# Kernel optimization log

Hardware: AMD Instinct MI355X
Metric: run time of the kernel (lower is better)

The kernel has to match this reference:

```python
import jax, jax.numpy as jnp
import numpy as np

T, B, F, H = 2048, 50, 750, 100  # time, batch(seen by LSTM), input feat, hidden
OUT = 2

def setup_inputs() -> dict:
    key = jax.random.key(0)
    ks = jax.random.split(key, 7)
    s = 1.0 / np.sqrt(H)
    u = lambda k, shape: jax.random.uniform(k, shape, jnp.float32, -s, s)
    return {
        "x": jax.random.normal(ks[0], (T, B, F), jnp.float32),
        "W_ih": u(ks[1], (4 * H, F)),
        "W_hh": u(ks[2], (4 * H, H)),
        "b_ih": u(ks[3], (4 * H,)),
        "b_hh": u(ks[4], (4 * H,)),
        "fc_W": u(ks[5], (OUT, B * H)),
        "fc_b": u(ks[6], (OUT,)),
    }

def reference(x, W_ih, W_hh, b_ih, b_hh, fc_W, fc_b):
    # PyTorch LSTM (batch_first=False): scan over dim0. Gate order: i, f, g, o.
    # Precompute input projections for all steps at once: (T, B, 4H)
    x_proj = jnp.einsum('tbf,gf->tbg', x, W_ih) + b_ih + b_hh

    def step(carry, xp):
        h, c = carry                      # (B, H) each
        gates = xp + h @ W_hh.T           # (B, 4H)
        i, f, g, o = jnp.split(gates, 4, axis=-1)
        i = jax.nn.sigmoid(i)
        f = jax.nn.sigmoid(f)
        g = jnp.tanh(g)
        o = jax.nn.sigmoid(o)
        c = f * c + i * g
        h = o * jnp.tanh(c)
        return (h, c), h

    h0 = jnp.zeros((B, H), x.dtype)
    c0 = jnp.zeros((B, H), x.dtype)
    _, hs = jax.lax.scan(step, (h0, c0), x_proj)  # hs: (T, B, H)
    flat = hs.reshape(hs.shape[0], -1)            # (T, B*H) == (T, 5000)
    return flat @ fc_W.T + fc_b                   # (T, 2)
```

## Files before the change

### kernel.cpp

```cpp
#include <hip/hip_runtime.h>

#define T_DIM 2048
#define B_DIM 50
#define F_DIM 750
#define H_DIM 100
#define G4    400
#define M_DIM (T_DIM * B_DIM)
#define KPAD  768

typedef __attribute__((ext_vector_type(8))) short short8v;
typedef __attribute__((ext_vector_type(4))) float f32x4;

__device__ __forceinline__ float fast_rcp(float x) { return __builtin_amdgcn_rcpf(x); }
__device__ __forceinline__ float sigm_f(float x) {
    return fast_rcp(1.0f + __expf(-x));
}
__device__ __forceinline__ float tanh_f(float x) {
    return 1.0f - 2.0f * fast_rcp(__expf(2.0f * x) + 1.0f);
}

__device__ __forceinline__ unsigned short f2bf_rne(float f) {
    unsigned int u = __float_as_uint(f);
    u = (u + 0x7FFFu + ((u >> 16) & 1u)) >> 16;
    return (unsigned short)u;
}
__device__ __forceinline__ float bf2f(unsigned short h) {
    return __uint_as_float(((unsigned int)h) << 16);
}

template <int CTRL>
__device__ __forceinline__ float qperm(float x) {
    return __int_as_float(__builtin_amdgcn_mov_dpp(__float_as_int(x), CTRL, 0xF, 0xF, false));
}

__global__ __launch_bounds__(256) void wconv(
    const float* __restrict__ W,
    unsigned short* __restrict__ Whi,
    unsigned short* __restrict__ Wlo)
{
    int i = blockIdx.x * 256 + threadIdx.x;
    if (i >= G4 * KPAD) return;
    int g = i / KPAD, k = i - g * KPAD;
    float v = (k < F_DIM) ? W[g * F_DIM + k] : 0.f;
    unsigned short h = f2bf_rne(v);
    Whi[i] = h;
    Wlo[i] = f2bf_rne(v - bf2f(h));
}

__global__ __launch_bounds__(256, 2) void xproj_mfma(
    const float* __restrict__ x,
    const unsigned short* __restrict__ Whi,
    const unsigned short* __restrict__ Wlo,
    const float* __restrict__ bih,
    const float* __restrict__ bhh,
    float* __restrict__ xp)
{
    const int m0   = blockIdx.x * 64;
    const int tid  = threadIdx.x;
    const int lane = tid & 63;
    const int w    = tid >> 6;
    const int fr   = lane & 15;
    const int fk   = (lane >> 4) * 8;

    __shared__ unsigned short Ahi[2][64][40];
    __shared__ unsigned short Alo[2][64][40];

    f32x4 acc[4][7];
    #pragma unroll
    for (int s = 0; s < 4; ++s)
        #pragma unroll
        for (int t = 0; t < 7; ++t)
            acc[s][t] = (f32x4){0.f, 0.f, 0.f, 0.f};

    float bias_t[7];
    #pragma unroll
    for (int tt = 0; tt < 7; ++tt) {
        const int nt = w + 4 * tt;
        if (nt < 25) {
            const int n = nt * 16 + fr;
            bias_t[tt] = bih[n] + bhh[n];
        } else bias_t[tt] = 0.f;
    }

    const int sr = tid >> 2;
    const int sc = (tid & 3) * 8;
    const float* xrow = x + (size_t)(m0 + sr) * F_DIM;

    float f[8];

    #define STAGE_LOAD(KS)                                                     \
    {                                                                          \
        const int kg = (KS) * 32 + sc;                                         \
        _Pragma("unroll")                                                      \
        for (int i = 0; i < 8; i += 2) {                                       \
            if (kg + i + 1 < F_DIM) {                                          \
                float2 v = *reinterpret_cast<const float2*>(&xrow[kg + i]);    \
                f[i] = v.x; f[i + 1] = v.y;                                    \
            } else {                                                           \
                f[i]     = (kg + i < F_DIM) ? xrow[kg + i] : 0.f;              \
                f[i + 1] = 0.f;                                                \
            }                                                                  \
        }                                                                      \
    }

    #define STAGE_WRITE(NB)                                                    \
    {                                                                          \
        short8v vh, vl;                                                        \
        _Pragma("unroll")                                                      \
        for (int i = 0; i < 8; ++i) {                                          \
            unsigned int u = __float_as_uint(f[i]);                            \
            vh[i] = (short)(u >> 16);                                          \
            float r = f[i] - __uint_as_float(u & 0xffff0000u);                 \
            vl[i] = (short)(__float_as_uint(r) >> 16);                         \
        }                                                                      \
        *reinterpret_cast<short8v*>(&Ahi[NB][sr][sc]) = vh;                    \
        *reinterpret_cast<short8v*>(&Alo[NB][sr][sc]) = vl;                    \
    }

    STAGE_LOAD(0);
    STAGE_WRITE(0);
    asm volatile("s_waitcnt lgkmcnt(0)\ns_barrier" ::: "memory");

    for (int s = 0; s < 24; ++s) {
        const int cur = s & 1;
        short8v ah[4], al[4];
        #pragma unroll
        for (int st = 0; st < 4; ++st) {
            ah[st] = *reinterpret_cast<const short8v*>(&Ahi[cur][st * 16 + fr][fk]);
            al[st] = *reinterpret_cast<const short8v*>(&Alo[cur][st * 16 + fr][fk]);
        }

        if (s < 23) STAGE_LOAD(s + 1);

        const int kb = s * 32 + fk;
        #pragma unroll
        for (int tt = 0; tt < 7; ++tt) {
            const int nt = w + 4 * tt;
            if (nt < 25) {
                const int n = nt * 16 + fr;
                const short8v bh = *reinterpret_cast<const short8v*>(&Whi[n * KPAD + kb]);
                const short8v bl = *reinterpret_cast<const short8v*>(&Wlo[n * KPAD + kb]);
                #pragma unroll
                for (int st = 0; st < 4; ++st) {
                    acc[st][tt] = __builtin_amdgcn_mfma_f32_16x16x32_bf16(ah[st], bh, acc[st][tt], 0, 0, 0);
                    acc[st][tt] = __builtin_amdgcn_mfma_f32_16x16x32_bf16(ah[st], bl, acc[st][tt], 0, 0, 0);
                    acc[st][tt] = __builtin_amdgcn_mfma_f32_16x16x32_bf16(al[st], bh, acc[st][tt], 0, 0, 0);
                }
            }
        }

        if (s < 23) STAGE_WRITE(cur ^ 1);
        asm volatile("s_waitcnt lgkmcnt(0)\ns_barrier" ::: "memory");
    }

    #pragma unroll
    for (int tt = 0; tt < 7; ++tt) {
        const int nt = w + 4 * tt;
        if (nt < 25) {
            const int n = nt * 16 + fr;
            #pragma unroll
            for (int st = 0; st < 4; ++st) {
                #pragma unroll
                for (int r = 0; r < 4; ++r) {
                    const int m = m0 + st * 16 + (lane >> 4) * 4 + r;
                    xp[(size_t)m * G4 + n] = acc[st][tt][r] + bias_t[tt];
                }
            }
        }
    }
    #undef STAGE_LOAD
    #undef STAGE_WRITE
}

__global__ __launch_bounds__(448, 1) void lstm_scan(
    const float* __restrict__ xp,
    const float* __restrict__ Whh,
    float* __restrict__ hs)
{
    const int b   = blockIdx.x;
    const int tid = threadIdx.x;
    const int q   = tid & 3;
    const int j   = tid >> 2;
    const int jc  = (j < H_DIM) ? j : (H_DIM - 1);
    const int row = q * H_DIM + jc;

    __shared__ __align__(16) float hbuf[2][112];

    float w[4][28];
    #pragma unroll
    for (int g = 0; g < 4; ++g) {
        const size_t base = (size_t)(g * H_DIM + jc) * H_DIM + 25 * q;
        #pragma unroll
        for (int r = 0; r < 25; ++r) w[g][r] = Whh[base + r];
        w[g][25] = w[g][26] = w[g][27] = 0.f;
    }
    if (tid < 112) { hbuf[0][tid] = 0.f; hbuf[1][tid] = 0.f; }

    const int hpos = (jc / 25) * 28 + (jc % 25);
    const bool writer = (q == 0) && (j < H_DIM);

    const float s_act = (q == 2) ? 2.0f : 1.0f;
    const float nsl2  = -s_act * 1.44269504088896f;
    const float nsm1  = 1.0f - s_act;

    float c = 0.f;
    const float* xp_ptr = xp + (size_t)b * G4 + row;
    float*       hs_ptr = hs + (size_t)b * H_DIM + j;
    float xpv = *xp_ptr;
    __syncthreads();

    int p = 0;
    for (int t = 0; t < T_DIM; ++t) {
        float xp_next = 0.f;
        if (t != T_DIM - 1) {
            xp_ptr += B_DIM * G4;
            xp_next = *xp_ptr;
        }

        float ac0 = (q == 0) ? xpv : 0.f;
        float ac1 = (q == 1) ? xpv : 0.f;
        float ac2 = (q == 2) ? xpv : 0.f;
        float ac3 = (q == 3) ? xpv : 0.f;
        #pragma unroll
        for (int k4 = 0; k4 < 7; ++k4) {
            float4 hv = *reinterpret_cast<const float4*>(&hbuf[p][28 * q + 4 * k4]);
            ac0 = fmaf(w[0][4 * k4 + 0], hv.x, ac0);
            ac0 = fmaf(w[0][4 * k4 + 1], hv.y, ac0);
            ac0 = fmaf(w[0][4 * k4 + 2], hv.z, ac0);
            ac0 = fmaf(w[0][4 * k4 + 3], hv.w, ac0);
            ac1 = fmaf(w[1][4 * k4 + 0], hv.x, ac1);
            ac1 = fmaf(w[1][4 * k4 + 1], hv.y, ac1);
            ac1 = fmaf(w[1][4 * k4 + 2], hv.z, ac1);
            ac1 = fmaf(w[1][4 * k4 + 3], hv.w, ac1);
            ac2 = fmaf(w[2][4 * k4 + 0], hv.x, ac2);
            ac2 = fmaf(w[2][4 * k4 + 1], hv.y, ac2);
            ac2 = fmaf(w[2][4 * k4 + 2], hv.z, ac2);
            ac2 = fmaf(w[2][4 * k4 + 3], hv.w, ac2);
            ac3 = fmaf(w[3][4 * k4 + 0], hv.x, ac3);
            ac3 = fmaf(w[3][4 * k4 + 1], hv.y, ac3);
            ac3 = fmaf(w[3][4 * k4 + 2], hv.z, ac3);
            ac3 = fmaf(w[3][4 * k4 + 3], hv.w, ac3);
        }
        ac0 += qperm<0xB1>(ac0);
        ac1 += qperm<0xB1>(ac1);
        ac2 += qperm<0xB1>(ac2);
        ac3 += qperm<0xB1>(ac3);
        ac0 += qperm<0x4E>(ac0);
        ac1 += qperm<0x4E>(ac1);
        ac2 += qperm<0x4E>(ac2);
        ac3 += qperm<0x4E>(ac3);

        float pre = ac0;
        pre = (q == 1) ? ac1 : pre;
        pre = (q == 2) ? ac2 : pre;
        pre = (q == 3) ? ac3 : pre;
        float act = fmaf(s_act, fast_rcp(1.0f + __builtin_amdgcn_exp2f(nsl2 * pre)), nsm1);

        float i_ = qperm<0x00>(act);
        float f_ = qperm<0x55>(act);
        float g_ = qperm<0xAA>(act);
        float o_ = qperm<0xFF>(act);

        c = fmaf(f_, c, i_ * g_);
        const float h = o_ * tanh_f(c);

        if (writer) {
            hbuf[p ^ 1][hpos] = h;
            *hs_ptr = h;
        }
        hs_ptr += B_DIM * H_DIM;
        asm volatile("s_waitcnt lgkmcnt(0)\ns_barrier" ::: "memory");
        p ^= 1;
        xpv = xp_next;
    }
}

__global__ __launch_bounds__(256) void fc_kernel(
    const float* __restrict__ hs,
    const float* __restrict__ fcW,
    const float* __restrict__ fcb,
    float* __restrict__ out)
{
    const int t   = blockIdx.x;
    const int tid = threadIdx.x;

    float p0 = 0.f, p1 = 0.f;
    for (int k = tid * 4; k < 5000; k += 1024) {
        const float4 hv = *reinterpret_cast<const float4*>(&hs[(size_t)t * 5000 + k]);
        const float4 w0 = *reinterpret_cast<const float4*>(&fcW[k]);
        const float4 w1 = *reinterpret_cast<const float4*>(&fcW[5000 + k]);
        p0 += hv.x * w0.x + hv.y * w0.y + hv.z * w0.z + hv.w * w0.w;
        p1 += hv.x * w1.x + hv.y * w1.y + hv.z * w1.z + hv.w * w1.w;
    }
    #pragma unroll
    for (int off = 32; off > 0; off >>= 1) {
        p0 += __shfl_xor(p0, off);
        p1 += __shfl_xor(p1, off);
    }
    __shared__ float red[8];
    const int wv = tid >> 6;
    if ((tid & 63) == 0) { red[wv * 2] = p0; red[wv * 2 + 1] = p1; }
    __syncthreads();
    if (tid == 0) {
        out[2 * t]     = fcb[0] + red[0] + red[2] + red[4] + red[6];
        out[2 * t + 1] = fcb[1] + red[1] + red[3] + red[5] + red[7];
    }
}

extern "C" void kernel_launch(void* const* d_in, const int* in_sizes, int n_in,
                              void* d_out, int out_size, void* d_ws, size_t ws_size,
                              hipStream_t stream) {
    const float* x   = (const float*)d_in[0];
    const float* Wih = (const float*)d_in[1];
    const float* Whh = (const float*)d_in[2];
    const float* bih = (const float*)d_in[3];
    const float* bhh = (const float*)d_in[4];
    const float* fcW = (const float*)d_in[5];
    const float* fcb = (const float*)d_in[6];
    float* out = (float*)d_out;

    char* ws = (char*)d_ws;
    float*          xp  = (float*)ws;
    unsigned short* Whi = (unsigned short*)(ws + (size_t)M_DIM * G4 * 4);
    unsigned short* Wlo = Whi + (size_t)G4 * KPAD;
    float*          hs  = (float*)((char*)(Wlo + (size_t)G4 * KPAD));

    wconv<<<(G4 * KPAD + 255) / 256, 256, 0, stream>>>(Wih, Whi, Wlo);

    xproj_mfma<<<M_DIM / 64, 256, 0, stream>>>(x, Whi, Wlo, bih, bhh, xp);

    lstm_scan<<<B_DIM, 448, 0, stream>>>(xp, Whh, hs);

    fc_kernel<<<T_DIM, 256, 0, stream>>>(hs, fcW, fcb, out);
}
```

Baseline: 1.493 ms.

## Enlarge xproj tile to 128 rows, pack LSTM scan FMAs, prefetch two steps

The input-projection GEMM now runs 512-thread blocks covering 128 rows, so two wave groups share each W_ih column tile. This halves the number of W reads per output row. The LSTM scan stores recurrent weights as float2 pairs and uses elementwise vector FMA, aiming at packed FP32 FMA instructions that shorten the serial per-step dot product. It also prefetches xp two timesteps ahead to hide global load latency on the recurrence. The larger GEMM block and the STAGE_LOAD indexing, which is partly hidden, must cover 128 rows correctly, and both changes raise register and LDS pressure.

```diff
diff --git a/kernel.cpp b/kernel.cpp
--- a/kernel.cpp
+++ b/kernel.cpp
@@ -10,11 +10,9 @@
 
 typedef __attribute__((ext_vector_type(8))) short short8v;
 typedef __attribute__((ext_vector_type(4))) float f32x4;
+typedef __attribute__((ext_vector_type(2))) float f32x2;
 
 __device__ __forceinline__ float fast_rcp(float x) { return __builtin_amdgcn_rcpf(x); }
-__device__ __forceinline__ float sigm_f(float x) {
-    return fast_rcp(1.0f + __expf(-x));
-}
 __device__ __forceinline__ float tanh_f(float x) {
     return 1.0f - 2.0f * fast_rcp(__expf(2.0f * x) + 1.0f);
 }
@@ -47,7 +45,7 @@
     Wlo[i] = f2bf_rne(v - bf2f(h));
 }
 
-__global__ __launch_bounds__(256, 2) void xproj_mfma(
+__global__ __launch_bounds__(512, 1) void xproj_mfma(
     const float* __restrict__ x,
     const unsigned short* __restrict__ Whi,
     const unsigned short* __restrict__ Wlo,
@@ -55,15 +53,17 @@
     const float* __restrict__ bhh,
     float* __restrict__ xp)
 {
-    const int m0   = blockIdx.x * 64;
+    const int m0   = blockIdx.x * 128;
     const int tid  = threadIdx.x;
     const int lane = tid & 63;
     const int w    = tid >> 6;
+    const int rb   = (w >> 2) * 64;
+    const int wc   = w & 3;
     const int fr   = lane & 15;
     const int fk   = (lane >> 4) * 8;
 
-    __shared__ unsigned short Ahi[2][64][40];
-    __shared__ unsigned short Alo[2][64][40];
+    __shared__ unsigned short Ahi[2][128][40];
+    __shared__ unsigned short Alo[2][128][40];
 
     f32x4 acc[4][7];
     #pragma unroll
@@ -75,7 +75,7 @@
     float bias_t[7];
     #pragma unroll
     for (int tt = 0; tt < 7; ++tt) {
-        const int nt = w + 4 * tt;
+        const int nt = wc + 4 * tt;
         if (nt < 25) {
             const int n = nt * 16 + fr;
             bias_t[tt] = bih[n] + bhh[n];
@@ -126,8 +126,8 @@
         short8v ah[4], al[4];
         #pragma unroll
         for (int st = 0; st < 4; ++st) {
-            ah[st] = *reinterpret_cast<const short8v*>(&Ahi[cur][st * 16 + fr][fk]);
-            al[st] = *reinterpret_cast<const short8v*>(&Alo[cur][st * 16 + fr][fk]);
+            ah[st] = *reinterpret_cast<const short8v*>(&Ahi[cur][rb + st * 16 + fr][fk]);
+            al[st] = *reinterpret_cast<const short8v*>(&Alo[cur][rb + st * 16 + fr][fk]);
         }
 
         if (s < 23) STAGE_LOAD(s + 1);
@@ -135,7 +135,7 @@
         const int kb = s * 32 + fk;
         #pragma unroll
         for (int tt = 0; tt < 7; ++tt) {
-            const int nt = w + 4 * tt;
+            const int nt = wc + 4 * tt;
             if (nt < 25) {
                 const int n = nt * 16 + fr;
                 const short8v bh = *reinterpret_cast<const short8v*>(&Whi[n * KPAD + kb]);
@@ -155,14 +155,14 @@
 
     #pragma unroll
     for (int tt = 0; tt < 7; ++tt) {
-        const int nt = w + 4 * tt;
+        const int nt = wc + 4 * tt;
         if (nt < 25) {
             const int n = nt * 16 + fr;
             #pragma unroll
             for (int st = 0; st < 4; ++st) {
                 #pragma unroll
                 for (int r = 0; r < 4; ++r) {
-                    const int m = m0 + st * 16 + (lane >> 4) * 4 + r;
+                    const int m = m0 + rb + st * 16 + (lane >> 4) * 4 + r;
                     xp[(size_t)m * G4 + n] = acc[st][tt][r] + bias_t[tt];
                 }
             }
@@ -186,14 +186,22 @@
 
     __shared__ __align__(16) float hbuf[2][112];
 
-    float w[4][28];
+    f32x2 w2[4][14];
     #pragma unroll
     for (int g = 0; g < 4; ++g) {
-        const size_t base = (size_t)(g * H_DIM + jc) * H_DIM + 25 * q;
-        #pragma unroll
-        for (int r = 0; r < 25; ++r) w[g][r] = Whh[base + r];
-        w[g][25] = w[g][26] = w[g][27] = 0.f;
-    }
+        const float* base = Whh + (size_t)(g * H_DIM + jc) * H_DIM + 25 * q;
+        #pragma unroll
+        for (int r = 0; r < 12; ++r)
+            w2[g][r] = (f32x2){base[2 * r], base[2 * r + 1]};
+        w2[g][12] = (f32x2){base[24], 0.f};
+        w2[g][13] = (f32x2){0.f, 0.f};
+    }
+    #pragma unroll
+    for (int g = 0; g < 4; ++g)
+        #pragma unroll
+        for (int r = 0; r < 14; ++r)
+            asm volatile("" : "+v"(w2[g][r]));
+
     if (tid < 112) { hbuf[0][tid] = 0.f; hbuf[1][tid] = 0.f; }
 
     const int hpos = (jc / 25) * 28 + (jc % 25);
@@ -206,41 +214,39 @@
     float c = 0.f;
     const float* xp_ptr = xp + (size_t)b * G4 + row;
     float*       hs_ptr = hs + (size_t)b * H_DIM + j;
-    float xpv = *xp_ptr;
+    const size_t xstride = (size_t)B_DIM * G4;
+
+    float xpv   = xp_ptr[0];
+    float xp_n1 = xp_ptr[xstride];
     __syncthreads();
 
     int p = 0;
     for (int t = 0; t < T_DIM; ++t) {
-        float xp_next = 0.f;
-        if (t != T_DIM - 1) {
-            xp_ptr += B_DIM * G4;
-            xp_next = *xp_ptr;
-        }
-
-        float ac0 = (q == 0) ? xpv : 0.f;
-        float ac1 = (q == 1) ? xpv : 0.f;
-        float ac2 = (q == 2) ? xpv : 0.f;
-        float ac3 = (q == 3) ? xpv : 0.f;
+        float xp_n2 = 0.f;
+        if (t + 2 < T_DIM) xp_n2 = xp_ptr[2 * xstride];
+        xp_ptr += xstride;
+
+        f32x2 a0 = {0.f, 0.f}, a1 = {0.f, 0.f}, a2 = {0.f, 0.f}, a3 = {0.f, 0.f};
+        const float* hq = &hbuf[p][28 * q];
         #pragma unroll
         for (int k4 = 0; k4 < 7; ++k4) {
-            float4 hv = *reinterpret_cast<const float4*>(&hbuf[p][28 * q + 4 * k4]);
-            ac0 = fmaf(w[0][4 * k4 + 0], hv.x, ac0);
-            ac0 = fmaf(w[0][4 * k4 + 1], hv.y, ac0);
-            ac0 = fmaf(w[0][4 * k4 + 2], hv.z, ac0);
-            ac0 = fmaf(w[0][4 * k4 + 3], hv.w, ac0);
-            ac1 = fmaf(w[1][4 * k4 + 0], hv.x, ac1);
-            ac1 = fmaf(w[1][4 * k4 + 1], hv.y, ac1);
-            ac1 = fmaf(w[1][4 * k4 + 2], hv.z, ac1);
-            ac1 = fmaf(w[1][4 * k4 + 3], hv.w, ac1);
-            ac2 = fmaf(w[2][4 * k4 + 0], hv.x, ac2);
-            ac2 = fmaf(w[2][4 * k4 + 1], hv.y, ac2);
-            ac2 = fmaf(w[2][4 * k4 + 2], hv.z, ac2);
-            ac2 = fmaf(w[2][4 * k4 + 3], hv.w, ac2);
-            ac3 = fmaf(w[3][4 * k4 + 0], hv.x, ac3);
-            ac3 = fmaf(w[3][4 * k4 + 1], hv.y, ac3);
-            ac3 = fmaf(w[3][4 * k4 + 2], hv.z, ac3);
-            ac3 = fmaf(w[3][4 * k4 + 3], hv.w, ac3);
-        }
+            float4 hv = *reinterpret_cast<const float4*>(hq + 4 * k4);
+            f32x2 hlo = {hv.x, hv.y};
+            f32x2 hhi = {hv.z, hv.w};
+            a0 = __builtin_elementwise_fma(w2[0][2 * k4],     hlo, a0);
+            a0 = __builtin_elementwise_fma(w2[0][2 * k4 + 1], hhi, a0);
+            a1 = __builtin_elementwise_fma(w2[1][2 * k4],     hlo, a1);
+            a1 = __builtin_elementwise_fma(w2[1][2 * k4 + 1], hhi, a1);
+            a2 = __builtin_elementwise_fma(w2[2][2 * k4],     hlo, a2);
+            a2 = __builtin_elementwise_fma(w2[2][2 * k4 + 1], hhi, a2);
+            a3 = __builtin_elementwise_fma(w2[3][2 * k4],     hlo, a3);
+            a3 = __builtin_elementwise_fma(w2[3][2 * k4 + 1], hhi, a3);
+        }
+        float ac0 = a0.x + a0.y + ((q == 0) ? xpv : 0.f);
+        float ac1 = a1.x + a1.y + ((q == 1) ? xpv : 0.f);
+        float ac2 = a2.x + a2.y + ((q == 2) ? xpv : 0.f);
+        float ac3 = a3.x + a3.y + ((q == 3) ? xpv : 0.f);
+
         ac0 += qperm<0xB1>(ac0);
         ac1 += qperm<0xB1>(ac1);
         ac2 += qperm<0xB1>(ac2);
@@ -271,7 +277,8 @@
         hs_ptr += B_DIM * H_DIM;
         asm volatile("s_waitcnt lgkmcnt(0)\ns_barrier" ::: "memory");
         p ^= 1;
-        xpv = xp_next;
+        xpv   = xp_n1;
+        xp_n1 = xp_n2;
     }
 }
 
@@ -327,7 +334,7 @@
 
     wconv<<<(G4 * KPAD + 255) / 256, 256, 0, stream>>>(Wih, Whi, Wlo);
 
-    xproj_mfma<<<M_DIM / 64, 256, 0, stream>>>(x, Whi, Wlo, bih, bhh, xp);
+    xproj_mfma<<<M_DIM / 128, 512, 0, stream>>>(x, Whi, Wlo, bih, bhh, xp);
 
     lstm_scan<<<B_DIM, 448, 0, stream>>>(xp, Whh, hs);
 
```

After: 1.664 ms. +11.5%, slower.
